# Kernel optimization log

Measured on AMD Instinct MI355X. Metric: run time of the kernel, lower is better.

## Reference

```python
import jax, jax.numpy as jnp
import numpy as np

EMBED_DIM = 200
INPUT_DIM = 512


def setup_inputs() -> dict:
    key = jax.random.key(0)
    k1, k2, k3, k4 = jax.random.split(key, 4)
    B, L, T = 64, 256, 64
    x = jax.random.normal(k1, (B, L, INPUT_DIM), dtype=jnp.float32)
    y = jax.random.normal(k2, (B, T, INPUT_DIM), dtype=jnp.float32)
    # fc = nn.Linear(input_dim, embedding_dim)
    W = jax.random.normal(k3, (EMBED_DIM, INPUT_DIM), dtype=jnp.float32) * (1.0 / np.sqrt(INPUT_DIM))
    b = jax.random.normal(k4, (EMBED_DIM,), dtype=jnp.float32) * 0.01
    return {"x": x, "y": y, "W": W, "b": b}


def reference(x, y, W, b):
    # Project both modalities (last dim != embedding_dim in original triggers fc)
    xp = jnp.einsum('bld,ed->ble', x, W) + b   # B x L x E
    yp = jnp.einsum('btd,ed->bte', y, W) + b   # B x T x E
    # Pairwise matchmap: for pair (i, j), matchmap = xp[i] @ yp[j].T -> L x T
    mm = jnp.einsum('ile,jte->ijlt', xp, yp)   # B x B x L x T
    # MISA: max over L (rows of matchmap, dim 0), then mean over T
    S = jnp.max(mm, axis=2).mean(axis=2)       # B x B
    return S
```

## Files before the change

kernel.cpp:

```cpp
#include <hip/hip_runtime.h>
#include <hip/hip_bf16.h>
#include <stdint.h>

#define BB 64
#define LL 256
#define TT 64
#define DD 512
#define EE 200
#define EP 208
#define NKK 13
#define NROWS_X 16384
#define YCH_PER_J (2 * NKK * 64)
#define BSTRIDE 264

typedef __attribute__((ext_vector_type(8))) short short8;
typedef __attribute__((ext_vector_type(4))) float floatx4;
typedef __attribute__((ext_vector_type(16))) float floatx16;
typedef __attribute__((ext_vector_type(4))) int intx4;

__device__ __forceinline__ short f2bf(float f) {
  uint32_t u = __builtin_bit_cast(uint32_t, f);
  u = (u + 0x7fffu + ((u >> 16) & 1u)) >> 16;
  return (short)u;
}

__device__ __forceinline__ uint32_t pack2(float lo, float hi) {
  return __builtin_amdgcn_perm(__builtin_bit_cast(uint32_t, hi),
                               __builtin_bit_cast(uint32_t, lo), 0x07060302u);
}

typedef const __attribute__((address_space(1))) uint32_t gu32_t;
typedef __attribute__((address_space(3))) uint32_t lu32_t;
__device__ __forceinline__ void glds16(const void* g, void* l) {
  __builtin_amdgcn_global_load_lds((gu32_t*)g, (lu32_t*)l, 16, 0, 0);
}

__global__ void wcvt_kernel(const float* __restrict__ W, short* __restrict__ Wb) {
  int idx = blockIdx.x * 256 + threadIdx.x;
  int e = idx >> 9;
  int k = idx & 511;
  float v = (e < EE) ? W[e * DD + k] : 0.0f;
  Wb[idx] = f2bf(v);
}

__global__ __launch_bounds__(256, 3) void proj_kernel(const float* __restrict__ x,
                                                      const float* __restrict__ y,
                                                      const short* __restrict__ Wb,
                                                      const float* __restrict__ bias,
                                                      short* __restrict__ pT) {
  __shared__ __align__(16) char smem[43008];
  float* ldsA = (float*)smem;
  short* ldsB = (short*)(smem + 16384);
  short* bounce = (short*)smem;

  const int tid  = threadIdx.x;
  const int lane = tid & 63;
  const int wid  = tid >> 6;
  const int r16   = lane & 15;
  const int khalf = lane >> 4;

  const int row0 = blockIdx.x * 64;
  const float* srcbase = (row0 < NROWS_X) ? (x + (size_t)row0 * DD)
                                          : (y + (size_t)(row0 - NROWS_X) * DD);

  floatx4 acc[NKK];
#pragma unroll
  for (int n = 0; n < NKK; n++) acc[n] = (floatx4){0.f, 0.f, 0.f, 0.f};

  auto stage = [&](int buf, int ks) {
#pragma unroll
    for (int it = 0; it < 2; it++) {
      const int p = it * 256 + tid;
      const int r = p >> 3, c = p & 7;
      glds16(srcbase + (size_t)r * DD + ks * 32 + ((c ^ (r & 7)) << 2),
             &ldsA[buf * 2048 + p * 4]);
    }
#pragma unroll
    for (int it = 0; it < 4; it++) {
      const int p = it * 256 + tid;
      if (p < 832) {
        const int r = p >> 2, c = p & 3;
        glds16(Wb + (size_t)r * DD + ks * 32 + ((c ^ (r & 3)) << 3),
               &ldsB[buf * 6656 + p * 8]);
      }
    }
  };

  stage(0, 0);

  for (int s = 0; s < 16; s++) {
    __syncthreads();
    if (s + 1 < 16) stage((s + 1) & 1, s + 1);

    const int buf = s & 1;
    const int r = wid * 16 + r16;
    const int c0 = (2 * khalf) ^ (r & 7);
    const int c1 = (2 * khalf + 1) ^ (r & 7);
    const floatx4 f0 = *(const floatx4*)&ldsA[buf * 2048 + r * 32 + c0 * 4];
    const floatx4 f1 = *(const floatx4*)&ldsA[buf * 2048 + r * 32 + c1 * 4];
    union { short8 s8; uint32_t u[4]; } af;
    af.u[0] = pack2(f0.x, f0.y);
    af.u[1] = pack2(f0.z, f0.w);
    af.u[2] = pack2(f1.x, f1.y);
    af.u[3] = pack2(f1.z, f1.w);
#pragma unroll
    for (int n = 0; n < NKK; n++) {
      const int erow = n * 16 + r16;
      const short8 bfrag = *(const short8*)&ldsB[buf * 6656 + erow * 32 + ((khalf ^ (erow & 3)) << 3)];
      acc[n] = __builtin_amdgcn_mfma_f32_16x16x32_bf16(af.s8, bfrag, acc[n], 0, 0, 0);
    }
  }

  __syncthreads();

#pragma unroll
  for (int n = 0; n < NKK; n++) {
    const int e = n * 16 + r16;
    const float bv = (e < EE) ? bias[e] : 0.0f;
#pragma unroll
    for (int rr = 0; rr < 4; rr++) {
      const int lr = wid * 16 + khalf * 4 + rr;
      bounce[lr * BSTRIDE + e] = f2bf(acc[n][rr] + bv);
    }
  }
  __syncthreads();

  const int rowblk0 = row0 >> 5;
  for (int c = tid; c < 1664; c += 256) {
    const int q  = c >> 6;
    const int mt = (q >= 13) ? 1 : 0;
    const int n  = q - mt * 13;
    const int l  = c & 63;
    const int lr = mt * 32 + (l & 31);
    const short8 piece = *(const short8*)&bounce[lr * BSTRIDE + n * 16 + (l >> 5) * 8];
    *(short8*)&pT[((size_t)((rowblk0 + mt) * 13 + n)) * 512 + l * 8] = piece;
  }
}

__global__ __launch_bounds__(512, 2) void pair_kernel(const short* __restrict__ xpT,
                                                      const short* __restrict__ ypT,
                                                      float* __restrict__ S) {
  __shared__ __align__(16) char ldsbuf[106496 + 16384];
  short* ylds = (short*)ldsbuf;
  float* red  = (float*)(ldsbuf + 106496);

  const int tid  = threadIdx.x;
  const int lane = tid & 63;
  const int wid  = tid >> 6;
  const int wq   = wid & 3;
  const int jh   = wid >> 2;
  const int ibase = (blockIdx.x >> 4) * 4;
  const int j0    = (blockIdx.x & 15) * 4;

  {
    const short* src = ypT + (size_t)j0 * YCH_PER_J * 8;
    for (int c = tid; c < 4 * YCH_PER_J; c += 512) {
      glds16(src + (size_t)c * 8, ldsbuf + c * 16);
    }
  }
  __syncthreads();

  for (int ii = 0; ii < 4; ii++) {
    const int i = ibase + ii;

    floatx16 acc[2][2][2];
#pragma unroll
    for (int jjj = 0; jjj < 2; jjj++)
#pragma unroll
      for (int m = 0; m < 2; m++)
#pragma unroll
        for (int nt = 0; nt < 2; nt++)
#pragma unroll
          for (int r = 0; r < 16; r++) acc[jjj][m][nt][r] = 0.f;

    const short* a0base = xpT + ((size_t)((i * 8 + wq * 2 + 0) * NKK) * 512) + lane * 8;
    const short* a1base = xpT + ((size_t)((i * 8 + wq * 2 + 1) * NKK) * 512) + lane * 8;

#pragma unroll
    for (int kk = 0; kk < NKK; kk++) {
      const short8 a0 = *(const short8*)(a0base + kk * 512);
      const short8 a1 = *(const short8*)(a1base + kk * 512);
#pragma unroll
      for (int jjj = 0; jjj < 2; jjj++) {
#pragma unroll
        for (int nt = 0; nt < 2; nt++) {
          const int jl = jh * 2 + jjj;
          const short8 bf = *(const short8*)(ylds + ((size_t)((jl * 2 + nt) * NKK + kk)) * 512 + lane * 8);
          acc[jjj][0][nt] = __builtin_amdgcn_mfma_f32_32x32x16_bf16(a0, bf, acc[jjj][0][nt], 0, 0, 0);
          acc[jjj][1][nt] = __builtin_amdgcn_mfma_f32_32x32x16_bf16(a1, bf, acc[jjj][1][nt], 0, 0, 0);
        }
      }
    }

#pragma unroll
    for (int jjj = 0; jjj < 2; jjj++) {
#pragma unroll
      for (int nt = 0; nt < 2; nt++) {
        float v = acc[jjj][0][nt][0];
#pragma unroll
        for (int m = 0; m < 2; m++)
#pragma unroll
          for (int r = 0; r < 16; r++) v = fmaxf(v, acc[jjj][m][nt][r]);
        v = fmaxf(v, __shfl_xor(v, 32, 64));
        if (lane < 32) {
          const int jl = jh * 2 + jjj;
          red[((wq * 4 + ii) * 4 + jl) * 64 + nt * 32 + lane] = v;
        }
      }
    }
  }
  __syncthreads();

#pragma unroll
  for (int w2 = 0; w2 < 2; w2++) {
    const int combo = wid * 2 + w2;
    const int ii = combo >> 2;
    const int jl = combo & 3;
    const int t  = lane;
    float v = red[((0 * 4 + ii) * 4 + jl) * 64 + t];
    v = fmaxf(v, red[((1 * 4 + ii) * 4 + jl) * 64 + t]);
    v = fmaxf(v, red[((2 * 4 + ii) * 4 + jl) * 64 + t]);
    v = fmaxf(v, red[((3 * 4 + ii) * 4 + jl) * 64 + t]);
    v += __shfl_xor(v, 1, 64);
    v += __shfl_xor(v, 2, 64);
    v += __shfl_xor(v, 4, 64);
    v += __shfl_xor(v, 8, 64);
    v += __shfl_xor(v, 16, 64);
    v += __shfl_xor(v, 32, 64);
    if (t == 0) S[(ibase + ii) * BB + j0 + jl] = v * (1.0f / 64.0f);
  }
}

extern "C" void kernel_launch(void* const* d_in, const int* in_sizes, int n_in,
                              void* d_out, int out_size, void* d_ws, size_t ws_size,
                              hipStream_t stream) {
  const float* x = (const float*)d_in[0];
  const float* y = (const float*)d_in[1];
  const float* W = (const float*)d_in[2];
  const float* b = (const float*)d_in[3];
  float* S = (float*)d_out;

  char* ws = (char*)d_ws;
  short* Wb = (short*)ws;
  short* pT = (short*)(ws + 262144);
  short* ypT = pT + (size_t)6656 * 512;

  wcvt_kernel<<<416, 256, 0, stream>>>(W, Wb);
  proj_kernel<<<320, 256, 0, stream>>>(x, y, Wb, b, pT);
  pair_kernel<<<256, 512, 0, stream>>>(pT, ypT, S);
}
```

Before: 48.94 us.

## Widen pair kernel to 16 waves, remap block order, vectorize W conversion

The pair kernel now launches 1024 threads per block. Each wave handles one 32-row L tile instead of two, which halves the accumulator registers per wave and doubles the wave count that shares each LDS copy of the y tiles. The block index is remapped so that consecutive blocks cover different i groups. The final reduction becomes an 8-way max, and the W bf16 conversion kernel processes 8 elements per thread with vector loads and stores. The trade-off is fewer MFMAs per A-fragment load and higher per-block thread and LDS usage. A 1024-thread block with about 139KB of LDS likely limits residency to one block per CU.

After: 63.64 us. +30.0%, slower.

```diff
diff --git a/kernel.cpp b/kernel.cpp
--- a/kernel.cpp
+++ b/kernel.cpp
@@ -16,7 +16,6 @@
 typedef __attribute__((ext_vector_type(8))) short short8;
 typedef __attribute__((ext_vector_type(4))) float floatx4;
 typedef __attribute__((ext_vector_type(16))) float floatx16;
-typedef __attribute__((ext_vector_type(4))) int intx4;
 
 __device__ __forceinline__ short f2bf(float f) {
   uint32_t u = __builtin_bit_cast(uint32_t, f);
@@ -36,11 +35,19 @@
 }
 
 __global__ void wcvt_kernel(const float* __restrict__ W, short* __restrict__ Wb) {
-  int idx = blockIdx.x * 256 + threadIdx.x;
-  int e = idx >> 9;
-  int k = idx & 511;
-  float v = (e < EE) ? W[e * DD + k] : 0.0f;
-  Wb[idx] = f2bf(v);
+  const int t = blockIdx.x * 256 + threadIdx.x;
+  const int base = t * 8;
+  const int e = base >> 9;
+  short8 o;
+  if (e < EE) {
+    const floatx4 f0 = *(const floatx4*)(W + base);
+    const floatx4 f1 = *(const floatx4*)(W + base + 4);
+    o[0] = f2bf(f0.x); o[1] = f2bf(f0.y); o[2] = f2bf(f0.z); o[3] = f2bf(f0.w);
+    o[4] = f2bf(f1.x); o[5] = f2bf(f1.y); o[6] = f2bf(f1.z); o[7] = f2bf(f1.w);
+  } else {
+    o = (short8)0;
+  }
+  *(short8*)(Wb + base) = o;
 }
 
 __global__ __launch_bounds__(256, 3) void proj_kernel(const float* __restrict__ x,
@@ -137,24 +144,27 @@
   }
 }
 
-__global__ __launch_bounds__(512, 2) void pair_kernel(const short* __restrict__ xpT,
-                                                      const short* __restrict__ ypT,
-                                                      float* __restrict__ S) {
-  __shared__ __align__(16) char ldsbuf[106496 + 16384];
+__global__ __launch_bounds__(1024, 4) void pair_kernel(const short* __restrict__ xpT,
+                                                       const short* __restrict__ ypT,
+                                                       float* __restrict__ S) {
+  __shared__ __align__(16) char ldsbuf[106496 + 32768];
   short* ylds = (short*)ldsbuf;
   float* red  = (float*)(ldsbuf + 106496);
 
   const int tid  = threadIdx.x;
   const int lane = tid & 63;
   const int wid  = tid >> 6;
-  const int wq   = wid & 3;
-  const int jh   = wid >> 2;
-  const int ibase = (blockIdx.x >> 4) * 4;
-  const int j0    = (blockIdx.x & 15) * 4;
+  const int lt   = wid & 7;
+  const int jh   = wid >> 3;
+  const int bid  = blockIdx.x;
+  const int igrp = ((bid & 7) << 1) | ((bid >> 3) & 1);
+  const int jgrp = bid >> 4;
+  const int ibase = igrp * 4;
+  const int j0    = jgrp * 4;
 
   {
     const short* src = ypT + (size_t)j0 * YCH_PER_J * 8;
-    for (int c = tid; c < 4 * YCH_PER_J; c += 512) {
+    for (int c = tid; c < 4 * YCH_PER_J; c += 1024) {
       glds16(src + (size_t)c * 8, ldsbuf + c * 16);
     }
   }
@@ -163,31 +173,26 @@
   for (int ii = 0; ii < 4; ii++) {
     const int i = ibase + ii;
 
-    floatx16 acc[2][2][2];
+    floatx16 acc[2][2];
 #pragma unroll
     for (int jjj = 0; jjj < 2; jjj++)
 #pragma unroll
-      for (int m = 0; m < 2; m++)
-#pragma unroll
-        for (int nt = 0; nt < 2; nt++)
-#pragma unroll
-          for (int r = 0; r < 16; r++) acc[jjj][m][nt][r] = 0.f;
-
-    const short* a0base = xpT + ((size_t)((i * 8 + wq * 2 + 0) * NKK) * 512) + lane * 8;
-    const short* a1base = xpT + ((size_t)((i * 8 + wq * 2 + 1) * NKK) * 512) + lane * 8;
+      for (int nt = 0; nt < 2; nt++)
+#pragma unroll
+        for (int r = 0; r < 16; r++) acc[jjj][nt][r] = 0.f;
+
+    const short* abase = xpT + ((size_t)((i * 8 + lt) * NKK) * 512) + lane * 8;
 
 #pragma unroll
     for (int kk = 0; kk < NKK; kk++) {
-      const short8 a0 = *(const short8*)(a0base + kk * 512);
-      const short8 a1 = *(const short8*)(a1base + kk * 512);
+      const short8 a = *(const short8*)(abase + kk * 512);
 #pragma unroll
       for (int jjj = 0; jjj < 2; jjj++) {
 #pragma unroll
         for (int nt = 0; nt < 2; nt++) {
           const int jl = jh * 2 + jjj;
           const short8 bf = *(const short8*)(ylds + ((size_t)((jl * 2 + nt) * NKK + kk)) * 512 + lane * 8);
-          acc[jjj][0][nt] = __builtin_amdgcn_mfma_f32_32x32x16_bf16(a0, bf, acc[jjj][0][nt], 0, 0, 0);
-          acc[jjj][1][nt] = __builtin_amdgcn_mfma_f32_32x32x16_bf16(a1, bf, acc[jjj][1][nt], 0, 0, 0);
+          acc[jjj][nt] = __builtin_amdgcn_mfma_f32_32x32x16_bf16(a, bf, acc[jjj][nt], 0, 0, 0);
         }
       }
     }
@@ -196,31 +201,27 @@
     for (int jjj = 0; jjj < 2; jjj++) {
 #pragma unroll
       for (int nt = 0; nt < 2; nt++) {
-        float v = acc[jjj][0][nt][0];
-#pragma unroll
-        for (int m = 0; m < 2; m++)
-#pragma unroll
-          for (int r = 0; r < 16; r++) v = fmaxf(v, acc[jjj][m][nt][r]);
+        float v = acc[jjj][nt][0];
+#pragma unroll
+        for (int r = 1; r < 16; r++) v = fmaxf(v, acc[jjj][nt][r]);
         v = fmaxf(v, __shfl_xor(v, 32, 64));
         if (lane < 32) {
           const int jl = jh * 2 + jjj;
-          red[((wq * 4 + ii) * 4 + jl) * 64 + nt * 32 + lane] = v;
+          red[((lt * 4 + ii) * 4 + jl) * 64 + nt * 32 + lane] = v;
         }
       }
     }
   }
   __syncthreads();
 
-#pragma unroll
-  for (int w2 = 0; w2 < 2; w2++) {
-    const int combo = wid * 2 + w2;
-    const int ii = combo >> 2;
-    const int jl = combo & 3;
+  {
+    const int ii = wid >> 2;
+    const int jl = wid & 3;
     const int t  = lane;
     float v = red[((0 * 4 + ii) * 4 + jl) * 64 + t];
-    v = fmaxf(v, red[((1 * 4 + ii) * 4 + jl) * 64 + t]);
-    v = fmaxf(v, red[((2 * 4 + ii) * 4 + jl) * 64 + t]);
-    v = fmaxf(v, red[((3 * 4 + ii) * 4 + jl) * 64 + t]);
+#pragma unroll
+    for (int l2 = 1; l2 < 8; l2++)
+      v = fmaxf(v, red[((l2 * 4 + ii) * 4 + jl) * 64 + t]);
     v += __shfl_xor(v, 1, 64);
     v += __shfl_xor(v, 2, 64);
     v += __shfl_xor(v, 4, 64);
@@ -245,7 +246,7 @@
   short* pT = (short*)(ws + 262144);
   short* ypT = pT + (size_t)6656 * 512;
 
-  wcvt_kernel<<<416, 256, 0, stream>>>(W, Wb);
+  wcvt_kernel<<<52, 256, 0, stream>>>(W, Wb);
   proj_kernel<<<320, 256, 0, stream>>>(x, y, Wb, b, pT);
-  pair_kernel<<<256, 512, 0, stream>>>(pT, ypT, S);
-}
+  pair_kernel<<<256, 1024, 0, stream>>>(pT, ypT, S);
+}
```
